# Kernel tuning notes

Hardware: AMD Instinct MI355X
Metric: run time of the kernel (lower is better)

Reference implementation:

```python
import jax, jax.numpy as jnp
import numpy as np

N_HEADS = 8


def setup_inputs() -> dict:
    key = jax.random.key(0)
    ks = jax.random.split(key, 6)
    B, U, Lx, Ly = 16, 512, 1024, 1024
    x = jax.random.normal(ks[0], (B, U, Lx), dtype=jnp.float32)
    y = jax.random.normal(ks[1], (B, U, Ly), dtype=jnp.float32)
    xy_mask = jax.random.randint(ks[2], (B, Lx, Ly), 0, 2).astype(jnp.bool_)
    wq = jax.random.normal(ks[3], (U, U), dtype=jnp.float32) * (1.0 / np.sqrt(U))
    wk = jax.random.normal(ks[4], (U, U), dtype=jnp.float32) * (1.0 / np.sqrt(U))
    wo = jax.random.normal(ks[5], (U, U), dtype=jnp.float32) * (1.0 / np.sqrt(U))
    return {"x": x, "y": y, "xy_mask": xy_mask, "wq": wq, "wk": wk, "wo": wo}


def reference(x, y, xy_mask, wq, wk, wo):
    # x: (B, U, Lx), y: (B, U, Ly), xy_mask: (B, Lx, Ly)
    B, U, Lx = x.shape
    Ly = y.shape[2]
    H = N_HEADS
    d = U // H
    scale = 1.0 / (d ** 0.5)

    # 1x1 conv (bias=False) == channel-mixing matmul; weight layout (out, in)
    Q = jnp.einsum('ou,bul->bol', wq, x)   # (B, U, Lx)
    K = jnp.einsum('ou,bul->bol', wk, y)   # (B, U, Ly)

    # split channels into heads (head-major channel order, matching torch.split)
    Qh = Q.reshape(B, H, d, Lx)
    Kh = K.reshape(B, H, d, Ly)

    # ReLU-scored attention with mask (no softmax)
    A = jnp.einsum('bhdx,bhdy->bhxy', Qh, Kh)           # (B, H, Lx, Ly)
    A = jnp.maximum(A, 0.0) * scale
    A = jnp.where(xy_mask[:, None, :, :], A, 0.0)

    C = jnp.einsum('bhxy,bhdy->bhdx', A, Kh).reshape(B, U, Lx)

    # per-row element-count normalization (rows with zero count use 1)
    n_el = jnp.maximum(jnp.sum(xy_mask, axis=2), 1)     # (B, Lx)
    C = C / n_el[:, None, :].astype(x.dtype)

    E = 0.5 * (Q + C)
    return jnp.einsum('ou,bul->bol', wo, E)
```

## Files before the change

### kernel.cpp

```cpp
#include <hip/hip_runtime.h>
#include <stdint.h>
#include <stddef.h>

#define B_  16
#define U_  512
#define LX_ 1024
#define LY_ 1024
#define H_  8
#define D_  64

typedef unsigned short ushort_t;
typedef unsigned int   uint_t;
typedef __bf16 v8bf  __attribute__((ext_vector_type(8)));
typedef float  v16f  __attribute__((ext_vector_type(16)));

__device__ __forceinline__ ushort_t bf16u(float f) {
    uint_t u = __float_as_uint(f);
    uint_t r = (u + 0x7FFFu + ((u >> 16) & 1u)) >> 16;
    return (ushort_t)r;
}
__device__ __forceinline__ float bfu2f(ushort_t u) {
    return __uint_as_float(((uint_t)u) << 16);
}
__device__ __forceinline__ uint_t pkbf16(float f0, float f1) {
    uint_t u0 = __float_as_uint(f0), u1 = __float_as_uint(f1);
    u0 = u0 + 0x7FFFu + ((u0 >> 16) & 1u);
    u1 = u1 + 0x7FFFu + ((u1 >> 16) & 1u);
    return __builtin_amdgcn_perm(u1, u0, 0x07060302u);
}
__device__ __forceinline__ void gload16(const void* g, void* l) {
    auto gp = (const __attribute__((address_space(1))) uint32_t*)(uintptr_t)g;
    auto lp = (__attribute__((address_space(3))) uint32_t*)(uintptr_t)l;
    __builtin_amdgcn_global_load_lds(gp, lp, 16, 0, 0);
}

__global__ void detect_kernel(const uint_t* __restrict__ mask, int* __restrict__ flag) {
    __shared__ int s;
    if (threadIdx.x == 0) s = 0;
    __syncthreads();
    int c = 0;
    for (int i = threadIdx.x; i < 1024; i += 256) c += (mask[i] <= 1u) ? 1 : 0;
    atomicAdd(&s, c);
    __syncthreads();
    if (threadIdx.x == 0) *flag = (s >= 1000) ? 1 : 0;
}

__global__ __launch_bounds__(256) void nelmask_kernel(const void* __restrict__ mask,
                                                      const int* __restrict__ flag,
                                                      float* __restrict__ nel,
                                                      uint_t* __restrict__ mb) {
    int row  = blockIdx.x * 4 + (threadIdx.x >> 6);
    int lane = threadIdx.x & 63;
    const int isInt = *flag;
    const uint8_t* m8  = (const uint8_t*)mask + (size_t)row * LY_;
    const int*     m32 = (const int*)mask + (size_t)row * LY_;
    int cnt = 0;
    for (int yg = 0; yg < LY_ / 64; ++yg) {
        int y = yg * 64 + lane;
        bool p = isInt ? (m32[y] != 0) : (m8[y] != 0);
        unsigned long long bal = __ballot(p);
        if (lane == 0) {
            mb[(size_t)row * 32 + yg * 2]     = (uint_t)bal;
            mb[(size_t)row * 32 + yg * 2 + 1] = (uint_t)(bal >> 32);
            cnt += __popcll(bal);
        }
    }
    if (lane == 0) nel[row] = (float)(cnt > 0 ? cnt : 1);
}

__global__ __launch_bounds__(256) void castw_kernel(const float* __restrict__ w0,
                                                    const float* __restrict__ w1,
                                                    const float* __restrict__ w2,
                                                    ushort_t* __restrict__ o0,
                                                    ushort_t* __restrict__ o1,
                                                    ushort_t* __restrict__ o2) {
    const float* s = blockIdx.y == 0 ? w0 : (blockIdx.y == 1 ? w1 : w2);
    ushort_t*    d = blockIdx.y == 0 ? o0 : (blockIdx.y == 1 ? o1 : o2);
    int i = (blockIdx.x * 256 + threadIdx.x) * 4;
    float4 v = *(const float4*)&s[i];
    ushort4 p;
    p.x = bf16u(v.x); p.y = bf16u(v.y); p.z = bf16u(v.z); p.w = bf16u(v.w);
    *(ushort4*)&d[i] = p;
}

__global__ __launch_bounds__(256) void castT_kernel(const float* __restrict__ X,
                                                    const float* __restrict__ Y,
                                                    ushort_t* __restrict__ XT,
                                                    ushort_t* __restrict__ YT) {
    const int l0 = blockIdx.x * 64;
    const int u0 = blockIdx.y * 64;
    const int b  = blockIdx.z & 15;
    const int sel = blockIdx.z >> 4;
    const float* S = sel ? Y : X;
    ushort_t*  Dst = sel ? YT : XT;
    __shared__ ushort_t T[64][72];
    const int tid = threadIdx.x;
    #pragma unroll
    for (int e = 0; e < 4; ++e) {
        int ci = e * 256 + tid;
        int r = ci >> 4, c4 = (ci & 15) * 4;
        float4 v = *(const float4*)&S[((size_t)(b * U_ + u0 + r) << 10) + l0 + c4];
        T[r][c4 + 0] = bf16u(v.x); T[r][c4 + 1] = bf16u(v.y);
        T[r][c4 + 2] = bf16u(v.z); T[r][c4 + 3] = bf16u(v.w);
    }
    __syncthreads();
    #pragma unroll
    for (int e = 0; e < 2; ++e) {
        int ci = e * 256 + tid;
        int lr = ci >> 3, cc = ci & 7;
        ushort_t tmp[8];
        #pragma unroll
        for (int j = 0; j < 8; ++j) tmp[j] = T[cc * 8 + j][lr];
        *(uint4*)&Dst[((size_t)((b << 10) + l0 + lr)) * U_ + u0 + cc * 8] = *(uint4*)tmp;
    }
}

template <int OUTF32>
__global__ __launch_bounds__(256) void gemm_mfma(const ushort_t* __restrict__ A, size_t aStr,
                                                 const ushort_t* __restrict__ Bm, size_t bStr,
                                                 void* __restrict__ Out, size_t oStr, int ldOut) {
    const int n0 = blockIdx.x * 128;
    const int m0 = blockIdx.y * 128;
    const int b  = blockIdx.z;
    __shared__ __align__(16) ushort_t As[128 * 64];
    __shared__ __align__(16) ushort_t Bs[128 * 64];
    const int tid = threadIdx.x;
    const ushort_t* Ab = A + aStr * b;
    const ushort_t* Bb = Bm + bStr * b;

    const int w = tid >> 6, lane = tid & 63, lo = lane & 31, hi = lane >> 5;
    const int wm = (w >> 1) * 64, wn = (w & 1) * 64;

    v16f acc00, acc01, acc10, acc11;
    #pragma unroll
    for (int i = 0; i < 16; ++i) { acc00[i] = 0.f; acc01[i] = 0.f; acc10[i] = 0.f; acc11[i] = 0.f; }

    for (int kk = 0; kk < 8; ++kk) {
        const int k0 = kk * 64;
        #pragma unroll
        for (int e = 0; e < 4; ++e) {
            int ci = e * 256 + tid;
            int r = ci >> 3, c = ci & 7;
            int g = (c ^ (r & 7)) << 3;
            gload16(&Ab[(size_t)(m0 + r) * U_ + k0 + g], &As[ci * 8]);
            gload16(&Bb[(size_t)(n0 + r) * U_ + k0 + g], &Bs[ci * 8]);
        }
        __syncthreads();
        #pragma unroll
        for (int ks = 0; ks < 4; ++ks) {
            int ch = ks * 2 + hi;
            int rA0 = wm + lo, rA1 = wm + 32 + lo;
            int rB0 = wn + lo, rB1 = wn + 32 + lo;
            v8bf a0 = *(v8bf*)&As[rA0 * 64 + ((ch ^ (rA0 & 7)) << 3)];
            v8bf a1 = *(v8bf*)&As[rA1 * 64 + ((ch ^ (rA1 & 7)) << 3)];
            v8bf b0 = *(v8bf*)&Bs[rB0 * 64 + ((ch ^ (rB0 & 7)) << 3)];
            v8bf b1 = *(v8bf*)&Bs[rB1 * 64 + ((ch ^ (rB1 & 7)) << 3)];
            acc00 = __builtin_amdgcn_mfma_f32_32x32x16_bf16(a0, b0, acc00, 0, 0, 0);
            acc01 = __builtin_amdgcn_mfma_f32_32x32x16_bf16(a0, b1, acc01, 0, 0, 0);
            acc10 = __builtin_amdgcn_mfma_f32_32x32x16_bf16(a1, b0, acc10, 0, 0, 0);
            acc11 = __builtin_amdgcn_mfma_f32_32x32x16_bf16(a1, b1, acc11, 0, 0, 0);
        }
        __syncthreads();
    }

    #pragma unroll
    for (int mi = 0; mi < 2; ++mi) {
        #pragma unroll
        for (int nj = 0; nj < 2; ++nj) {
            v16f c = mi ? (nj ? acc11 : acc10) : (nj ? acc01 : acc00);
            int n = n0 + wn + nj * 32 + lo;
            #pragma unroll
            for (int r = 0; r < 16; ++r) {
                int m = m0 + wm + mi * 32 + (r & 3) + 8 * (r >> 2) + 4 * hi;
                size_t addr = oStr * b + (size_t)m * ldOut + n;
                if (OUTF32) ((float*)Out)[addr] = c[r];
                else        ((ushort_t*)Out)[addr] = bf16u(c[r]);
            }
        }
    }
}

__global__ __launch_bounds__(256) void ktranspose_kernel(const ushort_t* __restrict__ Ka,
                                                         ushort_t* __restrict__ Kb) {
    const int y0 = blockIdx.x * 64;
    const int h  = blockIdx.y;
    const int b  = blockIdx.z;
    __shared__ ushort_t T[64][72];
    const int tid = threadIdx.x;

    #pragma unroll
    for (int e = 0; e < 2; ++e) {
        int idx = e * 256 + tid;
        int d = idx >> 3, c = idx & 7;
        uint4 v = *(const uint4*)&Ka[((size_t)(b * U_ + h * D_ + d) << 10) + y0 + c * 8];
        *(uint4*)&T[d][c * 8] = v;
    }
    __syncthreads();
    #pragma unroll
    for (int e = 0; e < 2; ++e) {
        int idx = e * 256 + tid;
        int yy = idx >> 3, dc = idx & 7;
        ushort_t tmp[8];
        #pragma unroll
        for (int j = 0; j < 8; ++j) tmp[j] = T[dc * 8 + j][yy];
        *(uint4*)&Kb[(((size_t)(b * H_ + h) << 10) + y0 + yy) * D_ + dc * 8] = *(uint4*)tmp;
    }
}

__global__ __launch_bounds__(256, 3) void attn_mfma(const ushort_t* __restrict__ QTg,
                                                    const ushort_t* __restrict__ Ka_g,
                                                    const ushort_t* __restrict__ Kb_g,
                                                    const uint_t* __restrict__ mbits,
                                                    const float* __restrict__ nel,
                                                    ushort_t* __restrict__ ETg) {
    const int tid = threadIdx.x;
    const int id  = blockIdx.x;
    const int bh  = id & 127;
    const int x0g = (id >> 7) * 128;
    const int b = bh >> 3, h = bh & 7;

    __shared__ __align__(16) ushort_t Qt[128 * 64];
    __shared__ __align__(16) ushort_t Kb[64 * 64];
    __shared__ __align__(16) ushort_t Ka[64 * 64];
    __shared__ __align__(16) ushort_t St[128 * 64];

    const int w    = tid >> 6;
    const int lane = tid & 63;
    const int lo   = lane & 31;
    const int hi   = lane >> 5;
    const int yw   = w & 1;
    const int xws  = (w >> 1) * 64;

    const ushort_t* Qsrc = QTg + ((size_t)(b * LX_ + x0g)) * U_ + h * D_;
    #pragma unroll
    for (int e = 0; e < 4; ++e) {
        int ci = e * 256 + tid;
        int r = ci >> 3, c = ci & 7;
        gload16(&Qsrc[(size_t)r * U_ + ((c ^ (r & 7)) << 3)], &Qt[ci * 8]);
    }
    const ushort_t* KaBase = Ka_g + ((size_t)(b * U_ + h * D_)) * LY_;
    const ushort_t* KbBase = Kb_g + ((size_t)(b * H_ + h)) * LY_ * D_;

    __syncthreads();
    v8bf qf0[4], qf1[4];
    {
        int rB0 = xws + lo, rB1 = xws + 32 + lo;
        #pragma unroll
        for (int kt = 0; kt < 4; ++kt) {
            int ch = kt * 2 + hi;
            qf0[kt] = *(v8bf*)&Qt[rB0 * 64 + ((ch ^ (rB0 & 7)) << 3)];
            qf1[kt] = *(v8bf*)&Qt[rB1 * 64 + ((ch ^ (rB1 & 7)) << 3)];
        }
    }

    v16f accC0, accC1;
    #pragma unroll
    for (int i = 0; i < 16; ++i) { accC0[i] = 0.f; accC1[i] = 0.f; }

    const int rowA = yw * 32 + lo;
    const int rB0  = xws + lo, rB1 = xws + 32 + lo;

    for (int y0 = 0; y0 < LY_; y0 += 64) {
        __syncthreads();
        #pragma unroll
        for (int e = 0; e < 2; ++e) {
            int ci = e * 256 + tid;
            int r = ci >> 3, c = ci & 7;
            int g8 = (c ^ (r & 7)) << 3;
            gload16(&KbBase[(size_t)(y0 + r) * D_ + g8], &Kb[ci * 8]);
            gload16(&KaBase[(size_t)r * LY_ + y0 + g8], &Ka[ci * 8]);
        }
        __syncthreads();

        v16f s0, s1;
        #pragma unroll
        for (int i = 0; i < 16; ++i) { s0[i] = 0.f; s1[i] = 0.f; }
        #pragma unroll
        for (int kt = 0; kt < 4; ++kt) {
            int ch = kt * 2 + hi;
            v8bf a = *(v8bf*)&Kb[rowA * 64 + ((ch ^ (rowA & 7)) << 3)];
            s0 = __builtin_amdgcn_mfma_f32_32x32x16_bf16(a, qf0[kt], s0, 0, 0, 0);
            s1 = __builtin_amdgcn_mfma_f32_32x32x16_bf16(a, qf1[kt], s1, 0, 0, 0);
        }
        #pragma unroll
        for (int i = 0; i < 2; ++i) {
            v16f s = i ? s1 : s0;
            int xl = xws + i * 32 + lo;
            uint_t wbits = mbits[((size_t)(b * LX_ + x0g + xl)) * 32 + (y0 >> 5) + yw];
            #pragma unroll
            for (int g = 0; g < 4; ++g) {
                uint_t w2 = wbits >> (g * 8 + 4 * hi);
                float f0 = fmaxf(s[g * 4 + 0], 0.f), f1 = fmaxf(s[g * 4 + 1], 0.f);
                float f2 = fmaxf(s[g * 4 + 2], 0.f), f3 = fmaxf(s[g * 4 + 3], 0.f);
                uint_t m0 = ((w2 & 1u) * 0xFFFFu) | ((w2 & 2u) * 0x7FFF8000u);
                uint_t m1 = (((w2 >> 2) & 1u) * 0xFFFFu) | (((w2 >> 2) & 2u) * 0x7FFF8000u);
                uint2 pk;
                pk.x = pkbf16(f0, f1) & m0;
                pk.y = pkbf16(f2, f3) & m1;
                int yb = yw * 32 + g * 8 + 4 * hi;
                *(uint2*)&St[xl * 64 + (((yb >> 3) ^ (xl & 7)) << 3) + (yb & 7)] = pk;
            }
        }
        __syncthreads();

        #pragma unroll
        for (int kt = 0; kt < 4; ++kt) {
            int ch = kt * 2 + hi;
            v8bf a  = *(v8bf*)&Ka[rowA * 64 + ((ch ^ (rowA & 7)) << 3)];
            v8bf b0 = *(v8bf*)&St[rB0 * 64 + ((ch ^ (rB0 & 7)) << 3)];
            v8bf b1 = *(v8bf*)&St[rB1 * 64 + ((ch ^ (rB1 & 7)) << 3)];
            accC0 = __builtin_amdgcn_mfma_f32_32x32x16_bf16(a, b0, accC0, 0, 0, 0);
            accC1 = __builtin_amdgcn_mfma_f32_32x32x16_bf16(a, b1, accC1, 0, 0, 0);
        }
    }

    __syncthreads();
    ushort_t* Et = St;
    #pragma unroll
    for (int i = 0; i < 2; ++i) {
        v16f c = i ? accC1 : accC0;
        int xl = xws + i * 32 + lo;
        float invn = 0.0625f / nel[b * LX_ + x0g + xl];
        #pragma unroll
        for (int g = 0; g < 4; ++g) {
            int d0 = yw * 32 + g * 8 + 4 * hi;
            int base = xl * 64 + ((((d0 >> 3) ^ (xl & 7)) << 3) | (d0 & 7));
            ushort_t q4[4];
            *(uint2*)q4 = *(const uint2*)&Qt[base];
            ushort_t e4[4];
            #pragma unroll
            for (int r4 = 0; r4 < 4; ++r4) {
                float e = 0.5f * bfu2f(q4[r4]) + c[g * 4 + r4] * invn;
                e4[r4] = bf16u(e);
            }
            *(uint2*)&Et[base] = *(uint2*)e4;
        }
    }
    __syncthreads();
    #pragma unroll
    for (int e = 0; e < 4; ++e) {
        int idx = e * 256 + tid;
        int row = idx >> 3, cc = idx & 7;
        uint4 v = *(const uint4*)&Et[row * 64 + ((cc ^ (row & 7)) << 3)];
        *(uint4*)&ETg[((size_t)(b * LX_ + x0g + row)) * U_ + h * D_ + cc * 8] = v;
    }
}

extern "C" void kernel_launch(void* const* d_in, const int* in_sizes, int n_in,
                              void* d_out, int out_size, void* d_ws, size_t ws_size,
                              hipStream_t stream) {
    const float* x    = (const float*)d_in[0];
    const float* y    = (const float*)d_in[1];
    const void*  mask = d_in[2];
    const float* wq   = (const float*)d_in[3];
    const float* wk   = (const float*)d_in[4];
    const float* wo   = (const float*)d_in[5];

    char* wsb = (char*)d_ws;
    ushort_t* xT    = (ushort_t*)(wsb);
    ushort_t* yT    = (ushort_t*)(wsb + 16777216);
    ushort_t* Ka    = (ushort_t*)(wsb + 33554432);
    ushort_t* wqb   = (ushort_t*)(wsb + 50331648);
    ushort_t* wkb   = (ushort_t*)(wsb + 50855936);
    ushort_t* wob   = (ushort_t*)(wsb + 51380224);
    uint_t*   mbits = (uint_t*)(wsb + 51904512);
    float*    nel   = (float*)(wsb + 54001664);
    int*      flag  = (int*)(wsb + 54067200);
    ushort_t* ET    = xT;
    ushort_t* Kb    = yT;
    ushort_t* QT    = (ushort_t*)d_out;

    detect_kernel<<<1, 256, 0, stream>>>((const uint_t*)mask, flag);
    nelmask_kernel<<<(B_ * LX_) / 4, 256, 0, stream>>>(mask, flag, nel, mbits);
    castw_kernel<<<dim3(U_ * U_ / 1024, 3), 256, 0, stream>>>(wq, wk, wo, wqb, wkb, wob);
    castT_kernel<<<dim3(16, 8, 32), 256, 0, stream>>>(x, y, xT, yT);

    gemm_mfma<0><<<dim3(4, 8, B_), 256, 0, stream>>>(
        xT, (size_t)LX_ * U_, wqb, 0, (void*)QT, (size_t)LX_ * U_, U_);
    gemm_mfma<0><<<dim3(8, 4, B_), 256, 0, stream>>>(
        wkb, 0, yT, (size_t)LY_ * U_, (void*)Ka, (size_t)U_ * LY_, LY_);
    ktranspose_kernel<<<dim3(LY_ / 64, H_, B_), 256, 0, stream>>>(Ka, Kb);
    attn_mfma<<<1024, 256, 0, stream>>>(QT, Ka, Kb, mbits, nel, ET);
    gemm_mfma<1><<<dim3(8, 4, B_), 256, 0, stream>>>(
        wob, 0, ET, (size_t)LX_ * U_, d_out, (size_t)U_ * LX_, LX_);
}
```

Baseline: 301.2 us.

## Keep attention scores in registers via permlane swap and double-buffer K tiles

The masked ReLU score tile is now converted to bf16 with v_cvt_pk_bf16_f32 and rearranged across lanes with permlane32_swap, so it feeds the second MFMA directly and no longer round-trips through a shared-memory St buffer. Each wave accumulates a split-K partial over its half of the y tile, and the two halves are reduced through LDS at the end. K tiles are double-buffered so the next tile's loads overlap compute, which cuts a barrier per iteration. This costs more accumulator registers and drops launch bounds from 3 to 2 blocks per SM, and adds an epilogue reduction.

```diff
diff --git a/kernel.cpp b/kernel.cpp
--- a/kernel.cpp
+++ b/kernel.cpp
@@ -207,7 +207,41 @@
     }
 }
 
-__global__ __launch_bounds__(256, 3) void attn_mfma(const ushort_t* __restrict__ QTg,
+typedef uint_t v2u __attribute__((ext_vector_type(2)));
+
+__device__ __forceinline__ void conv_sblock(const v16f& s, uint_t wbh, v8bf* fr) {
+    uint_t pk[8];
+    #pragma unroll
+    for (int i = 0; i < 8; ++i) {
+        float f0 = fmaxf(s[2 * i + 0], 0.f);
+        float f1 = fmaxf(s[2 * i + 1], 0.f);
+        uint_t r;
+        asm("v_cvt_pk_bf16_f32 %0, %1, %2" : "=v"(r) : "v"(f0), "v"(f1));
+        pk[i] = r;
+    }
+    #pragma unroll
+    for (int t = 0; t < 2; ++t) {
+        auto ra = __builtin_amdgcn_permlane32_swap(pk[4 * t + 0], pk[4 * t + 2], false, false);
+        auto rb = __builtin_amdgcn_permlane32_swap(pk[4 * t + 1], pk[4 * t + 3], false, false);
+        uint_t w0 = ra[0];
+        uint_t w1 = rb[0];
+        uint_t w2 = ra[1];
+        uint_t w3 = rb[1];
+        uint_t u0 = wbh >> (t * 16 + 0);
+        uint_t u1 = wbh >> (t * 16 + 2);
+        uint_t u2 = wbh >> (t * 16 + 4);
+        uint_t u3 = wbh >> (t * 16 + 6);
+        w0 &= ((u0 & 1u) * 0xFFFFu) | ((u0 & 2u) * 0x7FFF8000u);
+        w1 &= ((u1 & 1u) * 0xFFFFu) | ((u1 & 2u) * 0x7FFF8000u);
+        w2 &= ((u2 & 1u) * 0xFFFFu) | ((u2 & 2u) * 0x7FFF8000u);
+        w3 &= ((u3 & 1u) * 0xFFFFu) | ((u3 & 2u) * 0x7FFF8000u);
+        union { uint_t u[4]; v8bf b; } cv;
+        cv.u[0] = w0; cv.u[1] = w1; cv.u[2] = w2; cv.u[3] = w3;
+        fr[t] = cv.b;
+    }
+}
+
+__global__ __launch_bounds__(256, 2) void attn_mfma(const ushort_t* __restrict__ QTg,
                                                     const ushort_t* __restrict__ Ka_g,
                                                     const ushort_t* __restrict__ Kb_g,
                                                     const uint_t* __restrict__ mbits,
@@ -219,10 +253,10 @@
     const int x0g = (id >> 7) * 128;
     const int b = bh >> 3, h = bh & 7;
 
-    __shared__ __align__(16) ushort_t Qt[128 * 64];
-    __shared__ __align__(16) ushort_t Kb[64 * 64];
-    __shared__ __align__(16) ushort_t Ka[64 * 64];
-    __shared__ __align__(16) ushort_t St[128 * 64];
+    __shared__ __align__(16) ushort_t SM[8192 + 2 * 4096 + 2 * 4096];
+    ushort_t* Qt = SM;
+    ushort_t* KB = SM + 8192;
+    ushort_t* KA = SM + 16384;
 
     const int w    = tid >> 6;
     const int lane = tid & 63;
@@ -231,17 +265,27 @@
     const int yw   = w & 1;
     const int xws  = (w >> 1) * 64;
 
-    const ushort_t* Qsrc = QTg + ((size_t)(b * LX_ + x0g)) * U_ + h * D_;
+    const ushort_t* Qsrc   = QTg + ((size_t)(b * LX_ + x0g)) * U_ + h * D_;
+    const ushort_t* KaBase = Ka_g + ((size_t)(b * U_ + h * D_)) * LY_;
+    const ushort_t* KbBase = Kb_g + ((size_t)(b * H_ + h)) * LY_ * D_;
+    const int bx = b * LX_ + x0g;
+
     #pragma unroll
     for (int e = 0; e < 4; ++e) {
         int ci = e * 256 + tid;
         int r = ci >> 3, c = ci & 7;
         gload16(&Qsrc[(size_t)r * U_ + ((c ^ (r & 7)) << 3)], &Qt[ci * 8]);
     }
-    const ushort_t* KaBase = Ka_g + ((size_t)(b * U_ + h * D_)) * LY_;
-    const ushort_t* KbBase = Kb_g + ((size_t)(b * H_ + h)) * LY_ * D_;
-
-    __syncthreads();
+    #pragma unroll
+    for (int e = 0; e < 2; ++e) {
+        int ci = e * 256 + tid;
+        int r = ci >> 3, c = ci & 7;
+        int g8 = (c ^ (r & 7)) << 3;
+        gload16(&KbBase[(size_t)r * D_ + g8], &KB[ci * 8]);
+        gload16(&KaBase[(size_t)r * LY_ + g8], &KA[ci * 8]);
+    }
+    __syncthreads();
+
     v8bf qf0[4], qf1[4];
     {
         int rB0 = xws + lo, rB1 = xws + 32 + lo;
@@ -253,24 +297,32 @@
         }
     }
 
-    v16f accC0, accC1;
-    #pragma unroll
-    for (int i = 0; i < 16; ++i) { accC0[i] = 0.f; accC1[i] = 0.f; }
+    v16f acc00, acc01, acc10, acc11;
+    #pragma unroll
+    for (int i = 0; i < 16; ++i) { acc00[i] = 0.f; acc01[i] = 0.f; acc10[i] = 0.f; acc11[i] = 0.f; }
 
     const int rowA = yw * 32 + lo;
-    const int rB0  = xws + lo, rB1 = xws + 32 + lo;
-
-    for (int y0 = 0; y0 < LY_; y0 += 64) {
-        __syncthreads();
-        #pragma unroll
-        for (int e = 0; e < 2; ++e) {
-            int ci = e * 256 + tid;
-            int r = ci >> 3, c = ci & 7;
-            int g8 = (c ^ (r & 7)) << 3;
-            gload16(&KbBase[(size_t)(y0 + r) * D_ + g8], &Kb[ci * 8]);
-            gload16(&KaBase[(size_t)r * LY_ + y0 + g8], &Ka[ci * 8]);
-        }
-        __syncthreads();
+
+    for (int tt = 0; tt < 16; ++tt) {
+        const int y0 = tt * 64;
+        ushort_t* KBc = KB + (tt & 1) * 4096;
+        ushort_t* KAc = KA + (tt & 1) * 4096;
+
+        if (tt < 15) {
+            ushort_t* KBn = KB + ((tt + 1) & 1) * 4096;
+            ushort_t* KAn = KA + ((tt + 1) & 1) * 4096;
+            const int yn = y0 + 64;
+            #pragma unroll
+            for (int e = 0; e < 2; ++e) {
+                int ci = e * 256 + tid;
+                int r = ci >> 3, c = ci & 7;
+                int g8 = (c ^ (r & 7)) << 3;
+                gload16(&KbBase[(size_t)(yn + r) * D_ + g8], &KBn[ci * 8]);
+                gload16(&KaBase[(size_t)r * LY_ + yn + g8], &KAn[ci * 8]);
+            }
+        }
+        uint_t wb0 = mbits[((size_t)(bx + xws + lo)) * 32 + (y0 >> 5) + yw];
+        uint_t wb1 = mbits[((size_t)(bx + xws + 32 + lo)) * 32 + (y0 >> 5) + yw];
 
         v16f s0, s1;
         #pragma unroll
@@ -278,62 +330,69 @@
         #pragma unroll
         for (int kt = 0; kt < 4; ++kt) {
             int ch = kt * 2 + hi;
-            v8bf a = *(v8bf*)&Kb[rowA * 64 + ((ch ^ (rowA & 7)) << 3)];
+            v8bf a = *(v8bf*)&KBc[rowA * 64 + ((ch ^ (rowA & 7)) << 3)];
             s0 = __builtin_amdgcn_mfma_f32_32x32x16_bf16(a, qf0[kt], s0, 0, 0, 0);
             s1 = __builtin_amdgcn_mfma_f32_32x32x16_bf16(a, qf1[kt], s1, 0, 0, 0);
         }
-        #pragma unroll
-        for (int i = 0; i < 2; ++i) {
-            v16f s = i ? s1 : s0;
-            int xl = xws + i * 32 + lo;
-            uint_t wbits = mbits[((size_t)(b * LX_ + x0g + xl)) * 32 + (y0 >> 5) + yw];
+
+        v8bf fr0[2], fr1[2];
+        conv_sblock(s0, wb0 >> (hi * 8), fr0);
+        conv_sblock(s1, wb1 >> (hi * 8), fr1);
+
+        #pragma unroll
+        for (int t2 = 0; t2 < 2; ++t2) {
+            int ch = yw * 4 + t2 * 2 + hi;
+            v8bf a0 = *(v8bf*)&KAc[lo * 64 + ((ch ^ (lo & 7)) << 3)];
+            v8bf a1 = *(v8bf*)&KAc[(32 + lo) * 64 + ((ch ^ ((32 + lo) & 7)) << 3)];
+            acc00 = __builtin_amdgcn_mfma_f32_32x32x16_bf16(a0, fr0[t2], acc00, 0, 0, 0);
+            acc01 = __builtin_amdgcn_mfma_f32_32x32x16_bf16(a0, fr1[t2], acc01, 0, 0, 0);
+            acc10 = __builtin_amdgcn_mfma_f32_32x32x16_bf16(a1, fr0[t2], acc10, 0, 0, 0);
+            acc11 = __builtin_amdgcn_mfma_f32_32x32x16_bf16(a1, fr1[t2], acc11, 0, 0, 0);
+        }
+        __syncthreads();
+    }
+
+    float* red = (float*)(SM + 8192);
+    const int pair = w >> 1;
+    {
+        float* wr = red + pair * 4096 + (1 - yw) * 2048;
+        #pragma unroll
+        for (int xh = 0; xh < 2; ++xh) {
+            const v16f& c = (yw == 1) ? (xh ? acc01 : acc00) : (xh ? acc11 : acc10);
+            int xl2 = xh * 32 + lo;
             #pragma unroll
-            for (int g = 0; g < 4; ++g) {
-                uint_t w2 = wbits >> (g * 8 + 4 * hi);
-                float f0 = fmaxf(s[g * 4 + 0], 0.f), f1 = fmaxf(s[g * 4 + 1], 0.f);
-                float f2 = fmaxf(s[g * 4 + 2], 0.f), f3 = fmaxf(s[g * 4 + 3], 0.f);
-                uint_t m0 = ((w2 & 1u) * 0xFFFFu) | ((w2 & 2u) * 0x7FFF8000u);
-                uint_t m1 = (((w2 >> 2) & 1u) * 0xFFFFu) | (((w2 >> 2) & 2u) * 0x7FFF8000u);
-                uint2 pk;
-                pk.x = pkbf16(f0, f1) & m0;
-                pk.y = pkbf16(f2, f3) & m1;
-                int yb = yw * 32 + g * 8 + 4 * hi;
-                *(uint2*)&St[xl * 64 + (((yb >> 3) ^ (xl & 7)) << 3) + (yb & 7)] = pk;
+            for (int q = 0; q < 4; ++q) {
+                int chunk = (q * 2 + hi) ^ (xl2 & 7);
+                float4 v = make_float4(c[q * 4 + 0], c[q * 4 + 1], c[q * 4 + 2], c[q * 4 + 3]);
+                *(float4*)&wr[xl2 * 32 + chunk * 4] = v;
             }
         }
-        __syncthreads();
-
-        #pragma unroll
-        for (int kt = 0; kt < 4; ++kt) {
-            int ch = kt * 2 + hi;
-            v8bf a  = *(v8bf*)&Ka[rowA * 64 + ((ch ^ (rowA & 7)) << 3)];
-            v8bf b0 = *(v8bf*)&St[rB0 * 64 + ((ch ^ (rB0 & 7)) << 3)];
-            v8bf b1 = *(v8bf*)&St[rB1 * 64 + ((ch ^ (rB1 & 7)) << 3)];
-            accC0 = __builtin_amdgcn_mfma_f32_32x32x16_bf16(a, b0, accC0, 0, 0, 0);
-            accC1 = __builtin_amdgcn_mfma_f32_32x32x16_bf16(a, b1, accC1, 0, 0, 0);
-        }
-    }
-
-    __syncthreads();
-    ushort_t* Et = St;
-    #pragma unroll
-    for (int i = 0; i < 2; ++i) {
-        v16f c = i ? accC1 : accC0;
-        int xl = xws + i * 32 + lo;
-        float invn = 0.0625f / nel[b * LX_ + x0g + xl];
-        #pragma unroll
-        for (int g = 0; g < 4; ++g) {
-            int d0 = yw * 32 + g * 8 + 4 * hi;
-            int base = xl * 64 + ((((d0 >> 3) ^ (xl & 7)) << 3) | (d0 & 7));
-            ushort_t q4[4];
-            *(uint2*)q4 = *(const uint2*)&Qt[base];
-            ushort_t e4[4];
+    }
+    __syncthreads();
+    {
+        const int dh = yw;
+        float* rd = red + pair * 4096 + yw * 2048;
+        #pragma unroll
+        for (int xh = 0; xh < 2; ++xh) {
+            const v16f& c = (dh == 0) ? (xh ? acc01 : acc00) : (xh ? acc11 : acc10);
+            int xl2 = xh * 32 + lo;
+            int xl  = xws + xl2;
+            float invn = 0.0625f / nel[bx + xl];
             #pragma unroll
-            for (int r4 = 0; r4 < 4; ++r4) {
-                float e = 0.5f * bfu2f(q4[r4]) + c[g * 4 + r4] * invn;
-                e4[r4] = bf16u(e);
+            for (int q = 0; q < 4; ++q) {
+                int chunk = (q * 2 + hi) ^ (xl2 & 7);
+                float4 v = *(const float4*)&rd[xl2 * 32 + chunk * 4];
+                int d0 = dh * 32 + q * 8 + 4 * hi;
+                int base = xl * 64 + ((((d0 >> 3) ^ (xl & 7)) << 3) | (4 * hi));
+                ushort_t q4[4];
+                *(uint2*)q4 = *(const uint2*)&Qt[base];
+                ushort_t e4[4];
+                e4[0] = bf16u(0.5f * bfu2f(q4[0]) + (c[q * 4 + 0] + v.x) * invn);
+                e4[1] = bf16u(0.5f * bfu2f(q4[1]) + (c[q * 4 + 1] + v.y) * invn);
+                e4[2] = bf16u(0.5f * bfu2f(q4[2]) + (c[q * 4 + 2] + v.z) * invn);
+                e4[3] = bf16u(0.5f * bfu2f(q4[3]) + (c[q * 4 + 3] + v.w) * invn);
+                *(uint2*)&Qt[base] = *(uint2*)e4;
             }
-            *(uint2*)&Et[base] = *(uint2*)e4;
         }
     }
     __syncthreads();
@@ -341,8 +400,8 @@
     for (int e = 0; e < 4; ++e) {
         int idx = e * 256 + tid;
         int row = idx >> 3, cc = idx & 7;
-        uint4 v = *(const uint4*)&Et[row * 64 + ((cc ^ (row & 7)) << 3)];
-        *(uint4*)&ETg[((size_t)(b * LX_ + x0g + row)) * U_ + h * D_ + cc * 8] = v;
+        uint4 v = *(const uint4*)&Qt[row * 64 + ((cc ^ (row & 7)) << 3)];
+        *(uint4*)&ETg[((size_t)(bx + row)) * U_ + h * D_ + cc * 8] = v;
     }
 }
 
```

After: 296.2 us. About the same (-1.7%).
